# Optimization experiments

Measured on AMD Instinct MI355X. Metric: run time of the kernel, lower is better.

The kernel has to match this reference:

```python
import jax, jax.numpy as jnp
import numpy as np

N = 100000   # nodes
E = 1600000  # edges
F = 128      # feature / hidden dim
G = 512      # graphs in batch
L = 3        # conv layers
EPS = 1e-5   # batchnorm eps


def _gcn_conv(h, W, b, src, dst, dinv):
    # GCNConv: out = D^{-1/2} (A + I) D^{-1/2} (h W) + b
    hw = h @ W                                   # [N, F]
    norm = dinv[src] * dinv[dst]                 # [E]
    agg = jax.ops.segment_sum(hw[src] * norm[:, None], dst, num_segments=N)
    agg = agg + hw * (dinv * dinv)[:, None]      # self-loop contribution
    return agg + b


def _batchnorm(h, gamma, beta):
    # training-mode BN: batch statistics over the node dimension
    mu = h.mean(axis=0)
    var = h.var(axis=0)
    return gamma * (h - mu) * jax.lax.rsqrt(var + EPS) + beta


def setup_inputs() -> dict:
    key = jax.random.key(0)
    ks = jax.random.split(key, 8)
    x = jax.random.normal(ks[0], (N, F), dtype=jnp.float32)
    edge_index = jax.random.randint(ks[1], (2, E), 0, N)
    batch = jnp.sort(jax.random.randint(ks[2], (N,), 0, G))
    Ws = jax.random.normal(ks[3], (L, F, F), dtype=jnp.float32) / np.float32(np.sqrt(F))
    bs = jnp.zeros((L, F), jnp.float32)
    gammas = jnp.ones((L, F), jnp.float32)
    betas = jnp.zeros((L, F), jnp.float32)
    H = 64  # max(hidden//2, 16)
    w1 = jax.random.normal(ks[4], (2 * F, H), dtype=jnp.float32) / np.float32(np.sqrt(2 * F))
    b1 = jnp.zeros((H,), jnp.float32)
    w2 = jax.random.normal(ks[5], (H, 1), dtype=jnp.float32) / np.float32(np.sqrt(H))
    b2 = jnp.zeros((1,), jnp.float32)
    return dict(x=x, edge_index=edge_index, batch=batch, Ws=Ws, bs=bs,
                gammas=gammas, betas=betas, w1=w1, b1=b1, w2=w2, b2=b2)


def reference(x, edge_index, batch, Ws, bs, gammas, betas, w1, b1, w2, b2):
    src, dst = edge_index[0], edge_index[1]
    # symmetric gcn_norm degrees (self-loops included)
    deg = jax.ops.segment_sum(jnp.ones((E,), x.dtype), dst, num_segments=N) + 1.0
    dinv = jax.lax.rsqrt(deg)
    h = x
    for i in range(L):
        h = _gcn_conv(h, Ws[i], bs[i], src, dst, dinv)
        h = _batchnorm(h, gammas[i], betas[i])
        h = jax.nn.relu(h)  # dropout inactive (eval)
    counts = jax.ops.segment_sum(jnp.ones((N,), h.dtype), batch, num_segments=G)
    mean_pool = jax.ops.segment_sum(h, batch, num_segments=G) / jnp.maximum(counts, 1.0)[:, None]
    max_pool = jax.ops.segment_max(h, batch, num_segments=G)
    max_pool = jnp.where(jnp.isfinite(max_pool), max_pool, 0.0)  # empty segments -> 0
    z = jnp.concatenate([mean_pool, max_pool], axis=1)  # [G, 2F]
    z = jax.nn.relu(z @ w1 + b1)
    return z @ w2 + b2  # [G, 1]
```

## Files before the change

kernel.cpp:

```cpp
#include <hip/hip_runtime.h>
#include <hip/hip_fp16.h>


constexpr int F = 128;
constexpr float BN_EPS = 1e-5f;
constexpr int NB1 = 256;
constexpr int NBKT = 256;

typedef _Float16 f16x8 __attribute__((ext_vector_type(8)));
typedef float f32x4 __attribute__((ext_vector_type(4)));

__global__ __launch_bounds__(256) void part1_k(const int* __restrict__ dst, int* __restrict__ hist, int E) {
  __shared__ int cnt[NBKT];
  int tid = threadIdx.x;
  cnt[tid] = 0;
  __syncthreads();
  int chunk = (E + NB1 - 1) / NB1;
  int s = blockIdx.x * chunk, e = min(s + chunk, E);
  for (int i = s + tid; i < e; i += 256) atomicAdd(&cnt[dst[i] >> 9], 1);
  __syncthreads();
  hist[blockIdx.x * NBKT + tid] = cnt[tid];
}

__global__ __launch_bounds__(1024) void part_scan_k(const int* __restrict__ hist, int* __restrict__ base) {
  __shared__ int sh[1024];
  const int t = threadIdx.x;
  const int per = (NBKT * NB1) / 1024;
  int sum = 0;
  for (int j = 0; j < per; ++j) {
    int i = t * per + j;
    sum += hist[(i & (NB1 - 1)) * NBKT + (i >> 8)];
  }
  sh[t] = sum;
  __syncthreads();
  for (int off = 1; off < 1024; off <<= 1) {
    int v = (t >= off) ? sh[t - off] : 0;
    __syncthreads();
    sh[t] += v;
    __syncthreads();
  }
  int run = sh[t] - sum;
  for (int j = 0; j < per; ++j) {
    int i = t * per + j;
    int v = hist[(i & (NB1 - 1)) * NBKT + (i >> 8)];
    base[i] = run;
    run += v;
  }
}

__global__ __launch_bounds__(256) void part2_k(const int* __restrict__ src, const int* __restrict__ dst,
                                               const int* __restrict__ base, int2* __restrict__ pairbuf, int E) {
  __shared__ int cnt[NBKT];
  __shared__ int baseL[NBKT];
  int tid = threadIdx.x;
  cnt[tid] = 0;
  baseL[tid] = base[tid * NB1 + blockIdx.x];
  __syncthreads();
  int chunk = (E + NB1 - 1) / NB1;
  int s = blockIdx.x * chunk, e = min(s + chunk, E);
  for (int i = s + tid; i < e; i += 256) {
    int sv = src[i], dv = dst[i];
    int b = dv >> 9;
    int r = atomicAdd(&cnt[b], 1);
    pairbuf[baseL[b] + r] = make_int2(sv, dv);
  }
}

__global__ __launch_bounds__(256) void scat2_k(const int2* __restrict__ pairbuf, const int* __restrict__ base,
                                               int* __restrict__ rowptr, int* __restrict__ cols,
                                               float* __restrict__ dinv, int N, int E) {
  __shared__ int cnt[512];
  __shared__ int cur[512];
  __shared__ int ssum[256];
  const int b = blockIdx.x;
  const int tid = threadIdx.x;
  const int n0 = b << 9;
  cnt[tid] = 0; cnt[tid + 256] = 0;
  __syncthreads();
  const int lo = base[b * NB1];
  const int hi = (b == NBKT - 1) ? E : base[(b + 1) * NB1];
  for (int t = lo + tid; t < hi; t += 256)
    atomicAdd(&cnt[pairbuf[t].y - n0], 1);
  __syncthreads();
  const int c0 = cnt[2 * tid], c1 = cnt[2 * tid + 1];
  const int s = c0 + c1;
  ssum[tid] = s;
  __syncthreads();
  for (int off = 1; off < 256; off <<= 1) {
    int v = (tid >= off) ? ssum[tid - off] : 0;
    __syncthreads();
    ssum[tid] += v;
    __syncthreads();
  }
  const int excl = ssum[tid] - s;
  const int p0 = lo + excl, p1 = p0 + c0;
  const int node0 = n0 + 2 * tid, node1 = node0 + 1;
  if (node0 < N) { rowptr[node0] = p0; dinv[node0] = rsqrtf((float)c0 + 1.f); }
  if (node1 < N) { rowptr[node1] = p1; dinv[node1] = rsqrtf((float)c1 + 1.f); }
  cur[2 * tid] = p0; cur[2 * tid + 1] = p1;
  if (b == NBKT - 1 && tid == 255) rowptr[N] = E;
  __syncthreads();
  for (int t = lo + tid; t < hi; t += 256) {
    int2 pr = pairbuf[t];
    int pos = atomicAdd(&cur[pr.y - n0], 1);
    cols[pos] = pr.x;
  }
}

__global__ __launch_bounds__(128) void wprep_k(const float* __restrict__ W, __half* __restrict__ Wt) {
  const int b = blockIdx.x;
  const int k = threadIdx.x;
  const int l = b >> 7, c = b & 127;
  Wt[(size_t)b * 128 + k] = __float2half(W[(size_t)l * 16384 + k * 128 + c]);
}

__global__ void bnprep_k(const float* __restrict__ stats, const float* __restrict__ gamma,
                         const float* __restrict__ beta, float* __restrict__ scsh,
                         int first, float inv_n) {
  int c = threadIdx.x;
  if (first) { scsh[c] = 1.f; scsh[128 + c] = 0.f; return; }
  float mu = stats[c] * inv_n;
  float var = stats[128 + c] * inv_n - mu * mu;
  float sc = gamma[c] * rsqrtf(var + BN_EPS);
  scsh[c] = sc;
  scsh[128 + c] = beta[c] - mu * sc;
}

__global__ __launch_bounds__(256) void gemm_mfma_k(
    const float* __restrict__ Af, const __half* __restrict__ Ah,
    const __half* __restrict__ Wt, __half* __restrict__ Ch,
    const float* __restrict__ scsh, const float* __restrict__ dinv, int n, int dorelu) {
  __shared__ char Al[64 * 256];
  const int tid = threadIdx.x;
  const int r0 = blockIdx.x * 64;

  {
    const int row = tid & 63;
    const int cb = tid >> 6;
    const int r = r0 + row;
    const int c0 = cb * 32;
    float xv[32];
    if (Af) {
      if (r < n) {
        const float* ap = Af + (size_t)r * F + c0;
#pragma unroll
        for (int j = 0; j < 8; ++j) {
          float4 v = *(const float4*)(ap + j * 4);
          xv[4 * j] = v.x; xv[4 * j + 1] = v.y; xv[4 * j + 2] = v.z; xv[4 * j + 3] = v.w;
        }
      } else {
#pragma unroll
        for (int j = 0; j < 32; ++j) xv[j] = 0.f;
      }
    } else {
      if (r < n) {
        const int4* ap = (const int4*)(Ah + (size_t)r * F + c0);
#pragma unroll
        for (int j = 0; j < 4; ++j) {
          union { int4 q; __half2 h2[4]; } u;
          u.q = ap[j];
#pragma unroll
          for (int p = 0; p < 4; ++p) {
            float2 f = __half22float2(u.h2[p]);
            xv[8 * j + 2 * p] = f.x;
            xv[8 * j + 2 * p + 1] = f.y;
          }
        }
      } else {
#pragma unroll
        for (int j = 0; j < 32; ++j) xv[j] = 0.f;
      }
    }
    union { __half2 h2[16]; int4 q[4]; } u;
#pragma unroll
    for (int p = 0; p < 16; ++p) {
      float2 sc = *(const float2*)(scsh + c0 + 2 * p);
      float2 sh = *(const float2*)(scsh + 128 + c0 + 2 * p);
      float x0 = fmaf(xv[2 * p], sc.x, sh.x);
      float x1 = fmaf(xv[2 * p + 1], sc.y, sh.y);
      if (dorelu) { x0 = fmaxf(x0, 0.f); x1 = fmaxf(x1, 0.f); }
      u.h2[p] = __floats2half2_rn(x0, x1);
    }
    const int rowb = row * 256;
    const int swz = (row & 7) << 4;
#pragma unroll
    for (int j = 0; j < 4; ++j) {
      int off = (rowb + cb * 64 + j * 16) ^ swz;
      *(int4*)(Al + off) = u.q[j];
    }
  }
  __syncthreads();

  const int w = tid >> 6, l = tid & 63;
  const int arow = w * 16 + (l & 15);
  const int kg = l >> 4;
  f16x8 af[4];
  {
    const int swz = (arow & 7) << 4;
    const int base = arow * 256 + kg * 16;
#pragma unroll
    for (int kc = 0; kc < 4; ++kc)
      af[kc] = *(const f16x8*)(Al + ((base + kc * 64) ^ swz));
  }
  const int orow = r0 + w * 16 + kg * 4;
  float4 dvv = *(const float4*)(dinv + orow);
  float dvr[4] = {dvv.x, dvv.y, dvv.z, dvv.w};

#pragma unroll
  for (int t = 0; t < 8; ++t) {
    const __half* wp = Wt + ((size_t)(t * 16 + (l & 15)) * 128 + kg * 8);
    f32x4 acc = {0.f, 0.f, 0.f, 0.f};
#pragma unroll
    for (int kc = 0; kc < 4; ++kc) {
      f16x8 bf = *(const f16x8*)(wp + kc * 32);
      acc = __builtin_amdgcn_mfma_f32_16x16x32_f16(af[kc], bf, acc, 0, 0, 0);
    }
    const int ccol = t * 16 + (l & 15);
#pragma unroll
    for (int rr = 0; rr < 4; ++rr) {
      int r = orow + rr;
      if (r < n) Ch[(size_t)r * F + ccol] = __float2half(acc[rr] * dvr[rr]);
    }
  }
}

__global__ __launch_bounds__(256) void spmm_k(const __half* __restrict__ hw, const int* __restrict__ rowptr,
                                              const int* __restrict__ cols, const float* __restrict__ dinv,
                                              const float* __restrict__ bias, __half* __restrict__ outh, int n) {
  int wid = (blockIdx.x * 256 + threadIdx.x) >> 6;
  int lane = threadIdx.x & 63;
  if (wid >= n) return;
  const __half2* hw2 = (const __half2*)hw;
  float2 vf = __half22float2(hw2[(size_t)wid * 64 + lane]);
  float ax = vf.x, ay = vf.y;
  int j = rowptr[wid];
  const int e = rowptr[wid + 1];
  for (; j + 8 <= e; j += 8) {
    int c0 = cols[j + 0], c1 = cols[j + 1], c2 = cols[j + 2], c3 = cols[j + 3];
    int c4 = cols[j + 4], c5 = cols[j + 5], c6 = cols[j + 6], c7 = cols[j + 7];
    float2 v0 = __half22float2(hw2[(size_t)c0 * 64 + lane]);
    float2 v1 = __half22float2(hw2[(size_t)c1 * 64 + lane]);
    float2 v2 = __half22float2(hw2[(size_t)c2 * 64 + lane]);
    float2 v3 = __half22float2(hw2[(size_t)c3 * 64 + lane]);
    float2 v4 = __half22float2(hw2[(size_t)c4 * 64 + lane]);
    float2 v5 = __half22float2(hw2[(size_t)c5 * 64 + lane]);
    float2 v6 = __half22float2(hw2[(size_t)c6 * 64 + lane]);
    float2 v7 = __half22float2(hw2[(size_t)c7 * 64 + lane]);
    ax += ((v0.x + v1.x) + (v2.x + v3.x)) + ((v4.x + v5.x) + (v6.x + v7.x));
    ay += ((v0.y + v1.y) + (v2.y + v3.y)) + ((v4.y + v5.y) + (v6.y + v7.y));
  }
  if (j + 4 <= e) {
    int c0 = cols[j + 0], c1 = cols[j + 1], c2 = cols[j + 2], c3 = cols[j + 3];
    float2 v0 = __half22float2(hw2[(size_t)c0 * 64 + lane]);
    float2 v1 = __half22float2(hw2[(size_t)c1 * 64 + lane]);
    float2 v2 = __half22float2(hw2[(size_t)c2 * 64 + lane]);
    float2 v3 = __half22float2(hw2[(size_t)c3 * 64 + lane]);
    ax += (v0.x + v1.x) + (v2.x + v3.x);
    ay += (v0.y + v1.y) + (v2.y + v3.y);
    j += 4;
  }
  for (; j < e; ++j) {
    float2 vv = __half22float2(hw2[(size_t)cols[j] * 64 + lane]);
    ax += vv.x;
    ay += vv.y;
  }
  float di = dinv[wid];
  float2 b = ((const float2*)bias)[lane];
  ((__half2*)outh)[(size_t)wid * 64 + lane] =
      __floats2half2_rn(fmaf(di, ax, b.x), fmaf(di, ay, b.y));
}

__global__ __launch_bounds__(256) void stats16_k(const __half* __restrict__ h, float* __restrict__ stats, int n) {
  __shared__ float rs0[256], rs1[256], rq0[256], rq1[256];
  const int tid = threadIdx.x;
  const int c2 = tid & 63;
  const int rg = tid >> 6;
  const __half2* h2 = (const __half2*)h;
  float s0 = 0.f, s1 = 0.f, q0 = 0.f, q1 = 0.f;
  for (int r = blockIdx.x * 4 + rg; r < n; r += gridDim.x * 4) {
    float2 v = __half22float2(h2[(size_t)r * 64 + c2]);
    s0 += v.x; s1 += v.y;
    q0 += v.x * v.x; q1 += v.y * v.y;
  }
  rs0[tid] = s0; rs1[tid] = s1; rq0[tid] = q0; rq1[tid] = q1;
  __syncthreads();
  if (tid < 64) {
    atomicAdd(&stats[2 * tid], rs0[tid] + rs0[tid + 64] + rs0[tid + 128] + rs0[tid + 192]);
    atomicAdd(&stats[F + 2 * tid], rq0[tid] + rq0[tid + 64] + rq0[tid + 128] + rq0[tid + 192]);
  } else if (tid < 128) {
    const int l = tid - 64;
    atomicAdd(&stats[2 * l + 1], rs1[l] + rs1[l + 64] + rs1[l + 128] + rs1[l + 192]);
    atomicAdd(&stats[F + 2 * l + 1], rq1[l] + rq1[l + 64] + rq1[l + 128] + rq1[l + 192]);
  }
}

__global__ __launch_bounds__(256) void pool_mlp_k(
    const __half* __restrict__ h, const int* __restrict__ batch,
    const float* __restrict__ stats, const float* __restrict__ gamma,
    const float* __restrict__ beta, const float* __restrict__ w1,
    const float* __restrict__ b1, const float* __restrict__ w2,
    const float* __restrict__ b2, float* __restrict__ out,
    int n, float inv_n) {
  __shared__ float psum[4][128];
  __shared__ float pmax[4][128];
  __shared__ float zsh[256];
  __shared__ float part[4][64];
  const int g = blockIdx.x;
  const int tid = threadIdx.x;
  const int wave = tid >> 6, lane = tid & 63;

  int lo = 0, hi = n;
  while (lo < hi) { int m = (lo + hi) >> 1; if (batch[m] < g) lo = m + 1; else hi = m; }
  const int s = lo;
  hi = n;
  while (lo < hi) { int m = (lo + hi) >> 1; if (batch[m] < g + 1) lo = m + 1; else hi = m; }
  const int e = lo;

  const int c = lane * 2;
  float2 st = *(const float2*)(stats + c);
  float2 sq = *(const float2*)(stats + F + c);
  float2 ga = *(const float2*)(gamma + c);
  float2 be = *(const float2*)(beta + c);
  float mu0 = st.x * inv_n, mu1 = st.y * inv_n;
  float sc0 = ga.x * rsqrtf(sq.x * inv_n - mu0 * mu0 + BN_EPS);
  float sc1 = ga.y * rsqrtf(sq.y * inv_n - mu1 * mu1 + BN_EPS);
  float sh0 = be.x - mu0 * sc0;
  float sh1 = be.y - mu1 * sc1;

  const __half2* h2 = (const __half2*)h;
  float sum0 = 0.f, sum1 = 0.f, mx0 = 0.f, mx1 = 0.f;
#pragma unroll 2
  for (int r = s + wave; r < e; r += 4) {
    float2 v = __half22float2(h2[(size_t)r * 64 + lane]);
    float h0 = fmaxf(fmaf(v.x, sc0, sh0), 0.f);
    float h1 = fmaxf(fmaf(v.y, sc1, sh1), 0.f);
    sum0 += h0; sum1 += h1;
    mx0 = fmaxf(mx0, h0); mx1 = fmaxf(mx1, h1);
  }
  psum[wave][c] = sum0; psum[wave][c + 1] = sum1;
  pmax[wave][c] = mx0;  pmax[wave][c + 1] = mx1;
  __syncthreads();

  if (tid < 128) {
    float sm = psum[0][tid] + psum[1][tid] + psum[2][tid] + psum[3][tid];
    float mx = fmaxf(fmaxf(pmax[0][tid], pmax[1][tid]), fmaxf(pmax[2][tid], pmax[3][tid]));
    float ic = (e > s) ? 1.0f / (float)(e - s) : 0.f;
    zsh[tid] = sm * ic;
    zsh[128 + tid] = mx;
  }
  __syncthreads();

  {
    const int j = lane, q = wave;
    float acc = 0.f;
    const float* wq = w1 + (size_t)q * 64 * 64 + j;
#pragma unroll 8
    for (int i = 0; i < 64; ++i) acc = fmaf(zsh[q * 64 + i], wq[(size_t)i * 64], acc);
    part[q][j] = acc;
  }
  __syncthreads();

  if (tid < 64) {
    float hid = part[0][tid] + part[1][tid] + part[2][tid] + part[3][tid] + b1[tid];
    hid = fmaxf(hid, 0.f) * w2[tid];
    for (int off = 32; off > 0; off >>= 1) hid += __shfl_down(hid, off);
    if (tid == 0) out[g] = hid + b2[0];
  }
}

extern "C" void kernel_launch(void* const* d_in, const int* in_sizes, int n_in,
                              void* d_out, int out_size, void* d_ws, size_t ws_size,
                              hipStream_t stream) {
  const float* x      = (const float*)d_in[0];
  const int*   ei     = (const int*)d_in[1];
  const int*   batch  = (const int*)d_in[2];
  const float* Ws     = (const float*)d_in[3];
  const float* bsv    = (const float*)d_in[4];
  const float* gammas = (const float*)d_in[5];
  const float* betas  = (const float*)d_in[6];
  const float* w1     = (const float*)d_in[7];
  const float* b1     = (const float*)d_in[8];
  const float* w2     = (const float*)d_in[9];
  const float* b2     = (const float*)d_in[10];
  float* out = (float*)d_out;

  const int N = in_sizes[0] / F;
  const int E = in_sizes[1] / 2;
  const int G = out_size;
  const int L = in_sizes[3] / (F * F);
  const int* srcp = ei;
  const int* dstp = ei + E;

  char* p = (char*)d_ws;
  auto carve = [&](size_t bytes) {
    char* r = p;
    p += (bytes + 255) & ~(size_t)255;
    return r;
  };
  float*  dinv    = (float*)carve((size_t)N * 4);
  int*    rowptr  = (int*)carve(((size_t)N + 1) * 4);
  int*    colsb   = (int*)carve((size_t)E * 4);
  int*    hist    = (int*)carve((size_t)NB1 * NBKT * 4);
  int*    pbase   = (int*)carve((size_t)NB1 * NBKT * 4);
  int2*   pairbuf = (int2*)carve((size_t)E * 8);
  float*  bnstats = (float*)carve(2 * F * 4);
  float*  scsh    = (float*)carve(2 * F * 4);
  __half* wth     = (__half*)carve((size_t)L * F * F * 2);
  __half* hwh     = (__half*)carve((size_t)N * F * 2);
  __half* aggh    = (__half*)carve((size_t)N * F * 2);
  (void)ws_size; (void)n_in;

  part1_k<<<NB1, 256, 0, stream>>>(dstp, hist, E);
  part_scan_k<<<1, 1024, 0, stream>>>(hist, pbase);
  part2_k<<<NB1, 256, 0, stream>>>(srcp, dstp, pbase, pairbuf, E);
  scat2_k<<<NBKT, 256, 0, stream>>>(pairbuf, pbase, rowptr, colsb, dinv, N, E);
  wprep_k<<<L * F, 128, 0, stream>>>(Ws, wth);

  const float invN = 1.0f / (float)N;
  const int gblocks = (N + 63) / 64;
  for (int l = 0; l < L; ++l) {
    const float* ga = (l == 0) ? gammas : gammas + (size_t)(l - 1) * F;
    const float* be = (l == 0) ? betas : betas + (size_t)(l - 1) * F;
    bnprep_k<<<1, 128, 0, stream>>>(bnstats, ga, be, scsh, (l == 0) ? 1 : 0, invN);
    gemm_mfma_k<<<gblocks, 256, 0, stream>>>((l == 0) ? x : nullptr, (l == 0) ? nullptr : aggh,
                                             wth + (size_t)l * F * F, hwh, scsh, dinv, N,
                                             (l == 0) ? 0 : 1);
    hipMemsetAsync(bnstats, 0, 2 * F * 4, stream);
    spmm_k<<<(N * 64 + 255) / 256, 256, 0, stream>>>(hwh, rowptr, colsb, dinv,
                                                     bsv + (size_t)l * F, aggh, N);
    stats16_k<<<512, 256, 0, stream>>>(aggh, bnstats, N);
  }

  pool_mlp_k<<<G, 256, 0, stream>>>(aggh, batch, bnstats, gammas + (size_t)(L - 1) * F,
                                    betas + (size_t)(L - 1) * F, w1, b1, w2, b2, out, N, invN);
}
```

Before: 623.0 us.

## Fuse BN prep into stats kernel, stage weights in LDS, widen pooling

```diff
diff --git a/kernel.cpp b/kernel.cpp
--- a/kernel.cpp
+++ b/kernel.cpp
@@ -107,23 +107,18 @@
   }
 }
 
-__global__ __launch_bounds__(128) void wprep_k(const float* __restrict__ W, __half* __restrict__ Wt) {
+__global__ __launch_bounds__(128) void wprep_k(const float* __restrict__ W, __half* __restrict__ Wt,
+                                               float* __restrict__ scsh, float* __restrict__ stats,
+                                               int* __restrict__ ticket) {
   const int b = blockIdx.x;
   const int k = threadIdx.x;
   const int l = b >> 7, c = b & 127;
   Wt[(size_t)b * 128 + k] = __float2half(W[(size_t)l * 16384 + k * 128 + c]);
-}
-
-__global__ void bnprep_k(const float* __restrict__ stats, const float* __restrict__ gamma,
-                         const float* __restrict__ beta, float* __restrict__ scsh,
-                         int first, float inv_n) {
-  int c = threadIdx.x;
-  if (first) { scsh[c] = 1.f; scsh[128 + c] = 0.f; return; }
-  float mu = stats[c] * inv_n;
-  float var = stats[128 + c] * inv_n - mu * mu;
-  float sc = gamma[c] * rsqrtf(var + BN_EPS);
-  scsh[c] = sc;
-  scsh[128 + c] = beta[c] - mu * sc;
+  if (b == 0) {
+    scsh[k] = 1.f; scsh[128 + k] = 0.f;
+    stats[k] = 0.f; stats[128 + k] = 0.f;
+    if (k == 0) *ticket = 0;
+  }
 }
 
 __global__ __launch_bounds__(256) void gemm_mfma_k(
@@ -131,8 +126,17 @@
     const __half* __restrict__ Wt, __half* __restrict__ Ch,
     const float* __restrict__ scsh, const float* __restrict__ dinv, int n, int dorelu) {
   __shared__ char Al[64 * 256];
+  __shared__ char Wl[128 * 256];
   const int tid = threadIdx.x;
   const int r0 = blockIdx.x * 64;
+
+#pragma unroll
+  for (int j = 0; j < 8; ++j) {
+    int i = j * 256 + tid;
+    int c = i >> 4, q = i & 15;
+    int4 v = *(const int4*)((const char*)Wt + (size_t)i * 16);
+    *(int4*)(Wl + ((c * 256 + q * 16) ^ ((c & 7) << 4))) = v;
+  }
 
   {
     const int row = tid & 63;
@@ -208,11 +212,13 @@
 
 #pragma unroll
   for (int t = 0; t < 8; ++t) {
-    const __half* wp = Wt + ((size_t)(t * 16 + (l & 15)) * 128 + kg * 8);
+    const int bcol = t * 16 + (l & 15);
+    const int bswz = (bcol & 7) << 4;
+    const int bbase = bcol * 256 + kg * 16;
     f32x4 acc = {0.f, 0.f, 0.f, 0.f};
 #pragma unroll
     for (int kc = 0; kc < 4; ++kc) {
-      f16x8 bf = *(const f16x8*)(wp + kc * 32);
+      f16x8 bf = *(const f16x8*)(Wl + ((bbase + kc * 64) ^ bswz));
       acc = __builtin_amdgcn_mfma_f32_16x16x32_f16(af[kc], bf, acc, 0, 0, 0);
     }
     const int ccol = t * 16 + (l & 15);
@@ -270,8 +276,12 @@
       __floats2half2_rn(fmaf(di, ax, b.x), fmaf(di, ay, b.y));
 }
 
-__global__ __launch_bounds__(256) void stats16_k(const __half* __restrict__ h, float* __restrict__ stats, int n) {
+__global__ __launch_bounds__(256) void stats16_k(const __half* __restrict__ h, float* __restrict__ stats,
+                                                 const float* __restrict__ gamma, const float* __restrict__ beta,
+                                                 float* __restrict__ scsh, int* __restrict__ ticket,
+                                                 int n, float inv_n, int nblocks) {
   __shared__ float rs0[256], rs1[256], rq0[256], rq1[256];
+  __shared__ int amlast;
   const int tid = threadIdx.x;
   const int c2 = tid & 63;
   const int rg = tid >> 6;
@@ -292,19 +302,37 @@
     atomicAdd(&stats[2 * l + 1], rs1[l] + rs1[l + 64] + rs1[l + 128] + rs1[l + 192]);
     atomicAdd(&stats[F + 2 * l + 1], rq1[l] + rq1[l + 64] + rq1[l + 128] + rq1[l + 192]);
   }
-}
-
-__global__ __launch_bounds__(256) void pool_mlp_k(
+  __syncthreads();
+  if (tid == 0) {
+    __threadfence();
+    amlast = (atomicAdd(ticket, 1) == nblocks - 1);
+  }
+  __syncthreads();
+  if (amlast) {
+    if (tid < 128) {
+      float s = atomicAdd(&stats[tid], 0.f);
+      float q = atomicAdd(&stats[F + tid], 0.f);
+      float mu = s * inv_n;
+      float var = q * inv_n - mu * mu;
+      float sc = gamma[tid] * rsqrtf(var + BN_EPS);
+      scsh[tid] = sc;
+      scsh[128 + tid] = beta[tid] - mu * sc;
+    }
+    __syncthreads();
+    if (tid < 128) { stats[tid] = 0.f; stats[F + tid] = 0.f; }
+    if (tid == 0) *ticket = 0;
+  }
+}
+
+__global__ __launch_bounds__(512) void pool_mlp_k(
     const __half* __restrict__ h, const int* __restrict__ batch,
-    const float* __restrict__ stats, const float* __restrict__ gamma,
-    const float* __restrict__ beta, const float* __restrict__ w1,
+    const float* __restrict__ scsh, const float* __restrict__ w1,
     const float* __restrict__ b1, const float* __restrict__ w2,
-    const float* __restrict__ b2, float* __restrict__ out,
-    int n, float inv_n) {
-  __shared__ float psum[4][128];
-  __shared__ float pmax[4][128];
+    const float* __restrict__ b2, float* __restrict__ out, int n) {
+  __shared__ float psum[8][128];
+  __shared__ float pmax[8][128];
   __shared__ float zsh[256];
-  __shared__ float part[4][64];
+  __shared__ float part[8][64];
   const int g = blockIdx.x;
   const int tid = threadIdx.x;
   const int wave = tid >> 6, lane = tid & 63;
@@ -317,23 +345,16 @@
   const int e = lo;
 
   const int c = lane * 2;
-  float2 st = *(const float2*)(stats + c);
-  float2 sq = *(const float2*)(stats + F + c);
-  float2 ga = *(const float2*)(gamma + c);
-  float2 be = *(const float2*)(beta + c);
-  float mu0 = st.x * inv_n, mu1 = st.y * inv_n;
-  float sc0 = ga.x * rsqrtf(sq.x * inv_n - mu0 * mu0 + BN_EPS);
-  float sc1 = ga.y * rsqrtf(sq.y * inv_n - mu1 * mu1 + BN_EPS);
-  float sh0 = be.x - mu0 * sc0;
-  float sh1 = be.y - mu1 * sc1;
+  float2 sc = *(const float2*)(scsh + c);
+  float2 sh = *(const float2*)(scsh + 128 + c);
 
   const __half2* h2 = (const __half2*)h;
   float sum0 = 0.f, sum1 = 0.f, mx0 = 0.f, mx1 = 0.f;
 #pragma unroll 2
-  for (int r = s + wave; r < e; r += 4) {
+  for (int r = s + wave; r < e; r += 8) {
     float2 v = __half22float2(h2[(size_t)r * 64 + lane]);
-    float h0 = fmaxf(fmaf(v.x, sc0, sh0), 0.f);
-    float h1 = fmaxf(fmaf(v.y, sc1, sh1), 0.f);
+    float h0 = fmaxf(fmaf(v.x, sc.x, sh.x), 0.f);
+    float h1 = fmaxf(fmaf(v.y, sc.y, sh.y), 0.f);
     sum0 += h0; sum1 += h1;
     mx0 = fmaxf(mx0, h0); mx1 = fmaxf(mx1, h1);
   }
@@ -342,8 +363,12 @@
   __syncthreads();
 
   if (tid < 128) {
-    float sm = psum[0][tid] + psum[1][tid] + psum[2][tid] + psum[3][tid];
-    float mx = fmaxf(fmaxf(pmax[0][tid], pmax[1][tid]), fmaxf(pmax[2][tid], pmax[3][tid]));
+    float sm = 0.f, mx = 0.f;
+#pragma unroll
+    for (int q = 0; q < 8; ++q) {
+      sm += psum[q][tid];
+      mx = fmaxf(mx, pmax[q][tid]);
+    }
     float ic = (e > s) ? 1.0f / (float)(e - s) : 0.f;
     zsh[tid] = sm * ic;
     zsh[128 + tid] = mx;
@@ -353,15 +378,17 @@
   {
     const int j = lane, q = wave;
     float acc = 0.f;
-    const float* wq = w1 + (size_t)q * 64 * 64 + j;
+    const float* wq = w1 + (size_t)q * 32 * 64 + j;
 #pragma unroll 8
-    for (int i = 0; i < 64; ++i) acc = fmaf(zsh[q * 64 + i], wq[(size_t)i * 64], acc);
+    for (int i = 0; i < 32; ++i) acc = fmaf(zsh[q * 32 + i], wq[(size_t)i * 64], acc);
     part[q][j] = acc;
   }
   __syncthreads();
 
   if (tid < 64) {
-    float hid = part[0][tid] + part[1][tid] + part[2][tid] + part[3][tid] + b1[tid];
+    float hid = b1[tid];
+#pragma unroll
+    for (int q = 0; q < 8; ++q) hid += part[q][tid];
     hid = fmaxf(hid, 0.f) * w2[tid];
     for (int off = 32; off > 0; off >>= 1) hid += __shfl_down(hid, off);
     if (tid == 0) out[g] = hid + b2[0];
@@ -405,6 +432,7 @@
   int2*   pairbuf = (int2*)carve((size_t)E * 8);
   float*  bnstats = (float*)carve(2 * F * 4);
   float*  scsh    = (float*)carve(2 * F * 4);
+  int*    ticket  = (int*)carve(256);
   __half* wth     = (__half*)carve((size_t)L * F * F * 2);
   __half* hwh     = (__half*)carve((size_t)N * F * 2);
   __half* aggh    = (__half*)carve((size_t)N * F * 2);
@@ -414,23 +442,19 @@
   part_scan_k<<<1, 1024, 0, stream>>>(hist, pbase);
   part2_k<<<NB1, 256, 0, stream>>>(srcp, dstp, pbase, pairbuf, E);
   scat2_k<<<NBKT, 256, 0, stream>>>(pairbuf, pbase, rowptr, colsb, dinv, N, E);
-  wprep_k<<<L * F, 128, 0, stream>>>(Ws, wth);
+  wprep_k<<<L * F, 128, 0, stream>>>(Ws, wth, scsh, bnstats, ticket);
 
   const float invN = 1.0f / (float)N;
   const int gblocks = (N + 63) / 64;
   for (int l = 0; l < L; ++l) {
-    const float* ga = (l == 0) ? gammas : gammas + (size_t)(l - 1) * F;
-    const float* be = (l == 0) ? betas : betas + (size_t)(l - 1) * F;
-    bnprep_k<<<1, 128, 0, stream>>>(bnstats, ga, be, scsh, (l == 0) ? 1 : 0, invN);
     gemm_mfma_k<<<gblocks, 256, 0, stream>>>((l == 0) ? x : nullptr, (l == 0) ? nullptr : aggh,
                                              wth + (size_t)l * F * F, hwh, scsh, dinv, N,
                                              (l == 0) ? 0 : 1);
-    hipMemsetAsync(bnstats, 0, 2 * F * 4, stream);
     spmm_k<<<(N * 64 + 255) / 256, 256, 0, stream>>>(hwh, rowptr, colsb, dinv,
                                                      bsv + (size_t)l * F, aggh, N);
-    stats16_k<<<512, 256, 0, stream>>>(aggh, bnstats, N);
-  }
-
-  pool_mlp_k<<<G, 256, 0, stream>>>(aggh, batch, bnstats, gammas + (size_t)(L - 1) * F,
-                                    betas + (size_t)(L - 1) * F, w1, b1, w2, b2, out, N, invN);
-}
+    stats16_k<<<512, 256, 0, stream>>>(aggh, bnstats, gammas + (size_t)l * F,
+                                       betas + (size_t)l * F, scsh, ticket, N, invN, 512);
+  }
+
+  pool_mlp_k<<<G, 512, 0, stream>>>(aggh, batch, scsh, w1, b1, w2, b2, out, N);
+}
```

Result: faster. 582.3 us (-6.5%).
